# Kernel optimization log

Measured on AMD Instinct MI355X. Metric: run time of the kernel, lower is better.

The kernel has to match this reference:

```python
import jax, jax.numpy as jnp
import numpy as np

H, HKV, D, W = 64, 8, 64, 128          # heads, kv heads, head_dim, sliding window
G = H // HKV                            # query heads per kv head
HID = 2880
THETA = 150000.0
SCALE = D ** -0.5
NEG = -1e30


def _rope(x, positions):
    # x: [B,S,h,D]; GPT-NeoX style rotate_half RoPE
    half = D // 2
    inv_freq = 1.0 / (THETA ** (jnp.arange(0, half, dtype=jnp.float32) / half))
    ang = positions.astype(jnp.float32)[:, None] * inv_freq          # [S, D/2]
    cos = jnp.cos(ang)[None, :, None, :]
    sin = jnp.sin(ang)[None, :, None, :]
    x1, x2 = x[..., :half], x[..., half:]
    return jnp.concatenate([x1 * cos - x2 * sin, x2 * cos + x1 * sin], axis=-1)


def setup_inputs() -> dict:
    key = jax.random.key(0)
    ks = jax.random.split(key, 6)
    B, S = 1, 2048
    return {
        "hidden_states": jax.random.normal(ks[0], (B, S, HID), jnp.float32),
        "positions": jnp.arange(S, dtype=jnp.int32),
        "w_qkv": jax.random.normal(ks[1], (HID, (H + 2 * HKV) * D), jnp.float32) * 0.02,
        "b_qkv": jax.random.normal(ks[2], ((H + 2 * HKV) * D,), jnp.float32) * 0.02,
        "w_o": jax.random.normal(ks[3], (H * D, HID), jnp.float32) * 0.02,
        "b_o": jax.random.normal(ks[4], (HID,), jnp.float32) * 0.02,
        "sinks": jax.random.normal(ks[5], (H,), jnp.float32),
    }


def reference(hidden_states, positions, w_qkv, b_qkv, w_o, b_o, sinks):
    B, S, _ = hidden_states.shape
    qkv = hidden_states @ w_qkv + b_qkv                               # [B,S,(H+2Hkv)*D]
    q, k, v = jnp.split(qkv, [H * D, H * D + HKV * D], axis=-1)
    Q = q.reshape(B, S, H, D)
    K = k.reshape(B, S, HKV, D)
    V = v.reshape(B, S, HKV, D)
    Q = _rope(Q, positions)
    K = _rope(K, positions)

    # banded (sliding-window) key/value gather: query i sees keys i-W+1..i
    offsets = jnp.arange(W) - (W - 1)                                 # [-(W-1)..0]
    kidx = jnp.arange(S)[:, None] + offsets                           # [S,W]
    valid = kidx >= 0
    kidx = jnp.maximum(kidx, 0)
    Kw = K[:, kidx]                                                    # [B,S,W,HKV,D]
    Vw = V[:, kidx]

    Qr = Q.reshape(B, S, HKV, G, D)                                    # GQA grouping
    scores = jnp.einsum('bskgd,bswkd->bskgw', Qr, Kw) * SCALE          # [B,S,HKV,G,W]
    scores = jnp.where(valid[None, :, None, None, :], scores, NEG)

    sink = sinks.reshape(HKV, G)[None, None]                           # [1,1,HKV,G]
    m = jnp.maximum(scores.max(axis=-1), sink)                         # [B,S,HKV,G]
    p = jnp.exp(scores - m[..., None])
    denom = p.sum(axis=-1) + jnp.exp(sink - m)                         # sink in normalizer
    out = jnp.einsum('bskgw,bswkd->bskgd', p, Vw) / denom[..., None]

    out = out.reshape(B, S, H * D)
    return out @ w_o + b_o
```

## Files before the change

### kernel.cpp

```cpp
#include <hip/hip_runtime.h>

typedef unsigned short u16;
typedef __bf16 bf16x8 __attribute__((ext_vector_type(8)));
typedef float f32x4 __attribute__((ext_vector_type(4)));
typedef unsigned short u16x8 __attribute__((ext_vector_type(8)));

#define QKV_N 5120
#define SEQ 2048
#define ATTN_K 4096
#define KPAD 2944
#define SCALE 0.125f
#define NEGINF -1e30f

__device__ __forceinline__ u16 f2bf(float f) {
  unsigned int u = __builtin_bit_cast(unsigned int, f);
  u = (u + 0x7FFFu + ((u >> 16) & 1u)) >> 16;
  return (u16)u;
}

#define MFMA16(a, b, c) __builtin_amdgcn_mfma_f32_16x16x32_bf16((a), (b), (c), 0, 0, 0)

__device__ __forceinline__ void gl_lds16(const u16* g, u16* l) {
  __builtin_amdgcn_global_load_lds(
      (const __attribute__((address_space(1))) unsigned int*)(const void*)g,
      (__attribute__((address_space(3))) unsigned int*)(void*)l, 16, 0, 0);
}

__device__ __forceinline__ bf16x8 fragrd(const u16* base, int row, int rb) {
  return *(const bf16x8*)((const char*)(base + row * 32) + rb);
}

__device__ __forceinline__ bf16x8 lds_frag(const u16* mat, int row, int kh, int lg) {
  int off = row * 128 + ((kh * 64 + lg * 16) ^ ((row & 7) << 4));
  return *(const bf16x8*)((const char*)mat + off);
}

__global__ __launch_bounds__(256) void k_rope_table(const int* __restrict__ pos,
                                                    float2* __restrict__ tab) {
  int t = blockIdx.x * 256 + threadIdx.x;
  int s = t >> 5, i = t & 31;
  float freq = powf(150000.0f, -(float)i * (1.0f / 32.0f));
  float ang = (float)pos[s] * freq;
  float sv, cv;
  sincosf(ang, &sv, &cv);
  tab[t] = make_float2(cv, sv);
}

__global__ __launch_bounds__(256) void k_convert_pad(const float* __restrict__ in,
                                                     u16* __restrict__ out) {
  int i = blockIdx.x * 256 + threadIdx.x;
  int r = i / 736, c4 = i - r * 736;
  if (r >= 2048) return;
  ushort4 o = {0, 0, 0, 0};
  if (c4 < 720) {
    float4 v = *(const float4*)(in + (size_t)r * 2880 + c4 * 4);
    o.x = f2bf(v.x); o.y = f2bf(v.y); o.z = f2bf(v.z); o.w = f2bf(v.w);
  }
  ((ushort4*)out)[(size_t)r * 736 + c4] = o;
}

__global__ __launch_bounds__(256) void k_transpose(const float* __restrict__ in,
                                                   u16* __restrict__ out,
                                                   int Kin, int Kout, int Nd, int Npad) {
  __shared__ float tile[32][33];
  int n0 = blockIdx.x * 32, k0 = blockIdx.y * 32;
  int c = threadIdx.x & 31, r0 = threadIdx.x >> 5;
#pragma unroll
  for (int j = 0; j < 4; j++) {
    int r = r0 + j * 8;
    float v = 0.f;
    if (n0 + c < Nd && k0 + r < Kin) v = in[(size_t)(k0 + r) * Nd + n0 + c];
    tile[r][c] = v;
  }
  __syncthreads();
#pragma unroll
  for (int j = 0; j < 4; j++) {
    int rr = r0 + j * 8;
    int n = n0 + rr;
    if (n < Npad) out[(size_t)n * Kout + k0 + c] = f2bf(tile[c][rr]);
  }
}

__global__ __launch_bounds__(512, 1) void k_gemm1(const u16* __restrict__ Ag,
                                                  const u16* __restrict__ Bg,
                                                  const float* __restrict__ bias,
                                                  const float2* __restrict__ tab,
                                                  u16* __restrict__ C) {
  __shared__ u16 lds_[2][32768];
  u16* L = &lds_[0][0];
  const int tid = threadIdx.x;
  const int lane = tid & 63, wave = tid >> 6;
  const int wm = wave >> 2, wn = wave & 3;
  const int lr = lane & 15, lg = lane >> 4;
  int bid = blockIdx.x;
  int sb = (bid & 7) * 20 + (bid >> 3);
  const int m0 = (sb / 20) * 256, n0 = (sb % 20) * 256;

  f32x4 acc[8][4] = {};
  bf16x8 Bf[4];

  const int srow = wave * 16 + (lane >> 2);
  const int xsl = (((lane & 3) ^ ((lane >> 3) & 3)) << 3);
  const int rb = (lg * 16) ^ (((lr >> 1) & 3) << 4);

#define G1_STAGE_A(b, kh, kt)                                                   \
  { _Pragma("unroll") for (int r_ = 0; r_ < 2; r_++) {                          \
      gl_lds16(Ag + (size_t)(m0 + r_ * 128 + srow) * KPAD + (kt) + (kh) * 32 + xsl, \
               L + (b) * 32768 + (kh) * 8192 + (r_ * 128 + wave * 16) * 32); } }
#define G1_STAGE_B(b, kh, kt)                                                   \
  { _Pragma("unroll") for (int r_ = 0; r_ < 2; r_++) {                          \
      gl_lds16(Bg + (size_t)(n0 + r_ * 128 + srow) * KPAD + (kt) + (kh) * 32 + xsl, \
               L + (b) * 32768 + 16384 + (kh) * 8192 + (r_ * 128 + wave * 16) * 32); } }

#define VM4 asm volatile("s_waitcnt vmcnt(4)" ::: "memory");
#define VM0 asm volatile("s_waitcnt vmcnt(0)" ::: "memory");

#define PHASE(bb, kh, mh, LOADB, STAGE_STMT, WAIT_STMT)                         \
  {                                                                             \
    if (LOADB) {                                                                \
      _Pragma("unroll") for (int nf = 0; nf < 4; nf++)                          \
        Bf[nf] = fragrd(L + (bb) * 32768 + 16384 + (kh) * 8192,                 \
                        wn * 64 + nf * 16 + lr, rb);                            \
    }                                                                           \
    bf16x8 Af[4];                                                               \
    _Pragma("unroll") for (int mi = 0; mi < 4; mi++)                            \
      Af[mi] = fragrd(L + (bb) * 32768 + (kh) * 8192,                           \
                      wm * 128 + ((mh) * 4 + mi) * 16 + lr, rb);                \
    STAGE_STMT;                                                                 \
    WAIT_STMT;                                                                  \
    __builtin_amdgcn_s_barrier();                                               \
    __builtin_amdgcn_s_setprio(1);                                              \
    _Pragma("unroll") for (int mi = 0; mi < 4; mi++)                            \
      _Pragma("unroll") for (int nf = 0; nf < 4; nf++)                          \
        acc[(mh) * 4 + mi][nf] = MFMA16(Af[mi], Bf[nf], acc[(mh) * 4 + mi][nf]); \
    __builtin_amdgcn_s_setprio(0);                                              \
    __builtin_amdgcn_s_barrier();                                               \
  }

  G1_STAGE_A(0, 0, 0)
  G1_STAGE_B(0, 0, 0)
  G1_STAGE_A(0, 1, 0)
  G1_STAGE_B(0, 1, 0)
  VM4
  __builtin_amdgcn_s_barrier();

#define G1_ITER(ii, TAILV)                                                      \
  {                                                                             \
    const int ktB = (2 * (ii) + 1) * 64;                                        \
    const int ktC = (2 * (ii) + 2) * 64;                                        \
    PHASE(0, 0, 0, true,  { G1_STAGE_A(1, 0, ktB) }, {})                        \
    PHASE(0, 0, 1, false, { G1_STAGE_B(1, 0, ktB) }, VM4)                       \
    PHASE(0, 1, 0, true,  { G1_STAGE_A(1, 1, ktB) }, {})                        \
    PHASE(0, 1, 1, false, { G1_STAGE_B(1, 1, ktB) }, VM4)                       \
    PHASE(1, 0, 0, true,  { if (!(TAILV)) G1_STAGE_A(0, 0, ktC) }, {})          \
    PHASE(1, 0, 1, false, { if (!(TAILV)) G1_STAGE_B(0, 0, ktC) },              \
          { if (TAILV) { VM0 } else { VM4 } })                                  \
    PHASE(1, 1, 0, true,  { if (!(TAILV)) G1_STAGE_A(0, 1, ktC) }, {})          \
    PHASE(1, 1, 1, false, { if (!(TAILV)) G1_STAGE_B(0, 1, ktC) },              \
          { if (!(TAILV)) { VM4 } })                                            \
  }

  for (int i = 0; i < 22; i++) {
    G1_ITER(i, false)
  }
  G1_ITER(22, true)

#undef G1_ITER
#undef PHASE
#undef G1_STAGE_A
#undef G1_STAGE_B

  const bool rope = (n0 < 4608);
  if (rope) {
#pragma unroll
    for (int mf = 0; mf < 8; mf++)
#pragma unroll
      for (int nf = 0; nf < 2; nf++) {
        int col1 = n0 + wn * 64 + nf * 16 + lr;
        int col2 = col1 + 32;
        float b1 = bias[col1], b2 = bias[col2];
#pragma unroll
        for (int rg = 0; rg < 4; rg++) {
          int row = m0 + wm * 128 + mf * 16 + lg * 4 + rg;
          float2 cs = tab[(size_t)row * 32 + nf * 16 + lr];
          float x1 = acc[mf][nf][rg] + b1;
          float x2 = acc[mf][nf + 2][rg] + b2;
          C[(size_t)row * QKV_N + col1] = f2bf(x1 * cs.x - x2 * cs.y);
          C[(size_t)row * QKV_N + col2] = f2bf(x2 * cs.x + x1 * cs.y);
        }
      }
  } else {
#pragma unroll
    for (int mf = 0; mf < 8; mf++)
#pragma unroll
      for (int nf = 0; nf < 4; nf++) {
        int col = n0 + wn * 64 + nf * 16 + lr;
        float bv = bias[col];
#pragma unroll
        for (int rg = 0; rg < 4; rg++) {
          int row = m0 + wm * 128 + mf * 16 + lg * 4 + rg;
          C[(size_t)row * QKV_N + col] = f2bf(acc[mf][nf][rg] + bv);
        }
      }
  }
}

__global__ __launch_bounds__(256, 2) void k_gemm2(const u16* __restrict__ Ag,
                                                  const u16* __restrict__ Bg,
                                                  const float* __restrict__ bias,
                                                  float* __restrict__ C) {
  __shared__ u16 ldsbuf[2][16384];
  const int tid = threadIdx.x;
  const int lane = tid & 63, wave = tid >> 6;
  const int wm = wave >> 1, wn = wave & 1;
  const int lr = lane & 15, lg = lane >> 4;
  int bid = blockIdx.x;
  int sb = (bid & 7) * 46 + (bid >> 3);
  const int m0 = (sb / 23) * 128, n0 = (sb % 23) * 128;

  f32x4 acc[4][4] = {};

  const int srow = wave * 8 + (lane >> 3);
  const int sc = ((lane & 7) ^ (lane >> 3)) << 3;
  const u16* gA = Ag + (size_t)(m0 + srow) * ATTN_K + sc;
  const u16* gB = Bg + (size_t)(n0 + srow) * ATTN_K + sc;

#define G2_STAGE(kt, b)                                                          \
  {                                                                              \
    u16* Ab = &ldsbuf[b][0];                                                     \
    u16* Bb = &ldsbuf[b][8192];                                                  \
    _Pragma("unroll") for (int r = 0; r < 4; r++) {                              \
      gl_lds16(gA + (size_t)(r * 32) * ATTN_K + (kt), Ab + (r * 32 + wave * 8) * 64); \
      gl_lds16(gB + (size_t)(r * 32) * ATTN_K + (kt), Bb + (r * 32 + wave * 8) * 64); \
    }                                                                            \
  }

  G2_STAGE(0, 0)
  G2_STAGE(64, 1)
  asm volatile("s_waitcnt vmcnt(8)" ::: "memory");
  __builtin_amdgcn_s_barrier();

  for (int t = 0; t < 64; t++) {
    const int b = t & 1;
    const u16* La = &ldsbuf[b][0];
    const u16* Lb = &ldsbuf[b][8192];
    bf16x8 Bf[4][2];
#pragma unroll
    for (int nf = 0; nf < 4; nf++)
#pragma unroll
      for (int kh = 0; kh < 2; kh++)
        Bf[nf][kh] = lds_frag(Lb, wn * 64 + nf * 16 + lr, kh, lg);
    bf16x8 Af[2][2];
#pragma unroll
    for (int mi = 0; mi < 2; mi++)
#pragma unroll
      for (int kh = 0; kh < 2; kh++)
        Af[mi][kh] = lds_frag(La, wm * 64 + mi * 16 + lr, kh, lg);
#pragma unroll
    for (int q = 0; q < 2; q++) {
      bf16x8 An[2][2];
      if (q < 1) {
#pragma unroll
        for (int mi = 0; mi < 2; mi++)
#pragma unroll
          for (int kh = 0; kh < 2; kh++)
            An[mi][kh] = lds_frag(La, wm * 64 + ((q + 1) * 2 + mi) * 16 + lr, kh, lg);
      }
      __builtin_amdgcn_s_setprio(1);
#pragma unroll
      for (int mi = 0; mi < 2; mi++)
#pragma unroll
        for (int nf = 0; nf < 4; nf++)
#pragma unroll
          for (int kh = 0; kh < 2; kh++)
            acc[q * 2 + mi][nf] = MFMA16(Af[mi][kh], Bf[nf][kh], acc[q * 2 + mi][nf]);
      __builtin_amdgcn_s_setprio(0);
      if (q < 1) {
#pragma unroll
        for (int mi = 0; mi < 2; mi++)
#pragma unroll
          for (int kh = 0; kh < 2; kh++)
            Af[mi][kh] = An[mi][kh];
      }
    }
    __builtin_amdgcn_s_barrier();
    if (t <= 61) {
      G2_STAGE((t + 2) * 64, b)
      asm volatile("s_waitcnt vmcnt(8)" ::: "memory");
    } else {
      asm volatile("s_waitcnt vmcnt(0)" ::: "memory");
    }
    __builtin_amdgcn_s_barrier();
  }
#undef G2_STAGE

#pragma unroll
  for (int mi = 0; mi < 4; mi++)
#pragma unroll
    for (int ni = 0; ni < 4; ni++) {
      int row = m0 + wm * 64 + mi * 16 + lg * 4;
      int col = n0 + wn * 64 + ni * 16 + lr;
      if (col < 2880) {
        float bv = bias[col];
#pragma unroll
        for (int rg = 0; rg < 4; rg++)
          C[(size_t)(row + rg) * 2880 + col] = acc[mi][ni][rg] + bv;
      }
    }
}

__global__ __launch_bounds__(512, 2) void k_attn(const u16* __restrict__ qkv,
                                                 const float* __restrict__ sinks,
                                                 u16* __restrict__ out) {
  __shared__ u16 Klds[160 * 64];
  __shared__ u16 Vt[64 * 168];
  __shared__ u16 Pslab[8 * 32 * 40];
  const int hk = blockIdx.y;
  const int s0 = blockIdx.x * 32;
  const int kb = s0 - 127;
  const int tid = threadIdx.x;
  const int lane = tid & 63, w = tid >> 6;
  const int lr = lane & 15, lg = lane >> 4;

  for (int ch = tid; ch < 160 * 8; ch += 512) {
    int key = ch >> 3, c = ch & 7;
    int kidx = kb + key;
    u16x8 val = {0, 0, 0, 0, 0, 0, 0, 0};
    if (kidx >= 0 && kidx < SEQ)
      val = *(const u16x8*)(qkv + (size_t)kidx * QKV_N + 4096 + hk * 64 + c * 8);
    int off = (key * 128 + c * 16) ^ ((key & 7) << 4);
    *(u16x8*)((char*)Klds + off) = val;
  }
  for (int e4 = tid; e4 < 160 * 16; e4 += 512) {
    int key = e4 >> 4, d0 = (e4 & 15) * 4;
    int kidx = kb + key;
    ushort4 v = {0, 0, 0, 0};
    if (kidx >= 0 && kidx < SEQ)
      v = *(const ushort4*)(qkv + (size_t)kidx * QKV_N + 4608 + hk * 64 + d0);
    Vt[(d0 + 0) * 168 + key] = v.x;
    Vt[(d0 + 1) * 168 + key] = v.y;
    Vt[(d0 + 2) * 168 + key] = v.z;
    Vt[(d0 + 3) * 168 + key] = v.w;
  }

  const int head = hk * 8 + w;
  bf16x8 qf[2][2];
#pragma unroll
  for (int rt = 0; rt < 2; rt++)
#pragma unroll
    for (int ks = 0; ks < 2; ks++)
      qf[rt][ks] = *(const bf16x8*)(qkv + (size_t)(s0 + rt * 16 + lr) * QKV_N +
                                    head * 64 + ks * 32 + lg * 8);
  __syncthreads();

  f32x4 sc[2][10];
  f32x4 zz = {0.f, 0.f, 0.f, 0.f};
#pragma unroll
  for (int rt = 0; rt < 2; rt++)
#pragma unroll
    for (int nt = 0; nt < 10; nt++) sc[rt][nt] = zz;
#pragma unroll
  for (int nt = 0; nt < 10; nt++) {
    int key = nt * 16 + lr;
#pragma unroll
    for (int ks = 0; ks < 2; ks++) {
      int off = (key * 128 + ks * 64 + lg * 16) ^ ((key & 7) << 4);
      bf16x8 kf = *(const bf16x8*)((const char*)Klds + off);
      sc[0][nt] = MFMA16(qf[0][ks], kf, sc[0][nt]);
      sc[1][nt] = MFMA16(qf[1][ks], kf, sc[1][nt]);
    }
  }

#pragma unroll
  for (int rt = 0; rt < 2; rt++)
#pragma unroll
    for (int nt = 0; nt < 10; nt++)
#pragma unroll
      for (int rg = 0; rg < 4; rg++) {
        int qq = rt * 16 + lg * 4 + rg;
        int j = nt * 16 + lr;
        bool valid = (j >= qq) && (j <= qq + 127) && ((kb + j) >= 0);
        sc[rt][nt][rg] = valid ? sc[rt][nt][rg] * SCALE : NEGINF;
      }

  const float sink = sinks[head];
  float den[2][4];
#pragma unroll
  for (int rt = 0; rt < 2; rt++)
#pragma unroll
    for (int rg = 0; rg < 4; rg++) {
      float m = NEGINF;
#pragma unroll
      for (int nt = 0; nt < 10; nt++) m = fmaxf(m, sc[rt][nt][rg]);
#pragma unroll
      for (int x = 1; x < 16; x <<= 1) m = fmaxf(m, __shfl_xor(m, x, 64));
      m = fmaxf(m, sink);
      float sum = 0.f;
#pragma unroll
      for (int nt = 0; nt < 10; nt++) {
        float p = __expf(sc[rt][nt][rg] - m);
        sc[rt][nt][rg] = p;
        sum += p;
      }
#pragma unroll
      for (int x = 1; x < 16; x <<= 1) sum += __shfl_xor(sum, x, 64);
      den[rt][rg] = sum + __expf(sink - m);
    }

  f32x4 oacc[2][4];
#pragma unroll
  for (int rt = 0; rt < 2; rt++)
#pragma unroll
    for (int dn = 0; dn < 4; dn++) oacc[rt][dn] = zz;
  u16* slab = &Pslab[w * 32 * 40];
#pragma unroll
  for (int kt = 0; kt < 5; kt++) {
#pragma unroll
    for (int rt = 0; rt < 2; rt++)
#pragma unroll
      for (int j2 = 0; j2 < 2; j2++)
#pragma unroll
        for (int rg = 0; rg < 4; rg++)
          slab[(rt * 16 + lg * 4 + rg) * 40 + j2 * 16 + lr] = f2bf(sc[rt][kt * 2 + j2][rg]);
    asm volatile("s_waitcnt lgkmcnt(0)" ::: "memory");
    __builtin_amdgcn_sched_barrier(0);
    bf16x8 pf0 = *(const bf16x8*)&slab[lr * 40 + lg * 8];
    bf16x8 pf1 = *(const bf16x8*)&slab[(16 + lr) * 40 + lg * 8];
#pragma unroll
    for (int dn = 0; dn < 4; dn++) {
      bf16x8 vf = *(const bf16x8*)&Vt[(dn * 16 + lr) * 168 + kt * 32 + lg * 8];
      oacc[0][dn] = MFMA16(pf0, vf, oacc[0][dn]);
      oacc[1][dn] = MFMA16(pf1, vf, oacc[1][dn]);
    }
  }

#pragma unroll
  for (int rt = 0; rt < 2; rt++)
#pragma unroll
    for (int dn = 0; dn < 4; dn++)
#pragma unroll
      for (int rg = 0; rg < 4; rg++) {
        int s = s0 + rt * 16 + lg * 4 + rg;
        float val = oacc[rt][dn][rg] / den[rt][rg];
        out[(size_t)s * ATTN_K + head * 64 + dn * 16 + lr] = f2bf(val);
      }
}

extern "C" void kernel_launch(void* const* d_in, const int* in_sizes, int n_in,
                              void* d_out, int out_size, void* d_ws, size_t ws_size,
                              hipStream_t stream) {
  const float* hs = (const float*)d_in[0];
  const int* pos = (const int*)d_in[1];
  const float* wqkv = (const float*)d_in[2];
  const float* bqkv = (const float*)d_in[3];
  const float* wo = (const float*)d_in[4];
  const float* bo = (const float*)d_in[5];
  const float* sinks = (const float*)d_in[6];
  float* out = (float*)d_out;

  char* ws = (char*)d_ws;
  u16* qkvb = (u16*)(ws + 0);
  u16* hsb = (u16*)(ws + 41943040);
  u16* wqkvT = (u16*)(ws + 54001664);
  u16* attnb = (u16*)(ws + 41943040);
  u16* woT = (u16*)(ws + 84148224);
  float2* tab = (float2*)(ws + 108265472);

  k_rope_table<<<256, 256, 0, stream>>>(pos, tab);
  k_convert_pad<<<5888, 256, 0, stream>>>(hs, hsb);
  k_transpose<<<dim3(160, 92), 256, 0, stream>>>(wqkv, wqkvT, 2880, KPAD, 5120, 5120);
  k_transpose<<<dim3(92, 128), 256, 0, stream>>>(wo, woT, 4096, 4096, 2880, 2944);
  k_gemm1<<<160, 512, 0, stream>>>(hsb, wqkvT, bqkv, tab, qkvb);
  k_attn<<<dim3(64, 8), 512, 0, stream>>>(qkvb, sinks, attnb);
  k_gemm2<<<368, 256, 0, stream>>>(attnb, woT, bo, out);
}
```

Baseline: 202.2 us.

## Double-buffer LDS fragment reads in QKV GEMM to overlap with MFMAs

Restructures the QKV projection GEMM main loop so the A/B fragments for the next phase are read from LDS into alternating register sets while the current phase's MFMAs run. Before, each phase read its fragments and then immediately consumed them. The global-to-LDS staging and vmcnt waits are also regrouped, with A and B issued together in some phases. This is meant to hide LDS read latency behind matrix-core work. The cost is roughly double the fragment registers, plus a more intricate barrier and wait ordering that must stay correct.

```diff
diff --git a/kernel.cpp b/kernel.cpp
--- a/kernel.cpp
+++ b/kernel.cpp
@@ -97,7 +97,7 @@
   const int m0 = (sb / 20) * 256, n0 = (sb % 20) * 256;
 
   f32x4 acc[8][4] = {};
-  bf16x8 Bf[4];
+  bf16x8 AfA[4], AfB[4], BfA[4], BfB[4];
 
   const int srow = wave * 16 + (lane >> 2);
   const int xsl = (((lane & 3) ^ ((lane >> 3) & 3)) << 3);
@@ -115,24 +115,25 @@
 #define VM4 asm volatile("s_waitcnt vmcnt(4)" ::: "memory");
 #define VM0 asm volatile("s_waitcnt vmcnt(0)" ::: "memory");
 
-#define PHASE(bb, kh, mh, LOADB, STAGE_STMT, WAIT_STMT)                         \
+#define PREF_A(dst, bb, kh, mh)                                                 \
+  _Pragma("unroll") for (int mi = 0; mi < 4; mi++)                              \
+    dst[mi] = fragrd(L + (bb) * 32768 + (kh) * 8192,                            \
+                     wm * 128 + ((mh) * 4 + mi) * 16 + lr, rb);
+#define PREF_B(dst, bb, kh)                                                     \
+  _Pragma("unroll") for (int nf = 0; nf < 4; nf++)                              \
+    dst[nf] = fragrd(L + (bb) * 32768 + 16384 + (kh) * 8192,                    \
+                     wn * 64 + nf * 16 + lr, rb);
+
+#define PH(STAGE_STMT, WAIT_STMT, PREF_STMT, mh, AFS, BFS)                      \
   {                                                                             \
-    if (LOADB) {                                                                \
-      _Pragma("unroll") for (int nf = 0; nf < 4; nf++)                          \
-        Bf[nf] = fragrd(L + (bb) * 32768 + 16384 + (kh) * 8192,                 \
-                        wn * 64 + nf * 16 + lr, rb);                            \
-    }                                                                           \
-    bf16x8 Af[4];                                                               \
-    _Pragma("unroll") for (int mi = 0; mi < 4; mi++)                            \
-      Af[mi] = fragrd(L + (bb) * 32768 + (kh) * 8192,                           \
-                      wm * 128 + ((mh) * 4 + mi) * 16 + lr, rb);                \
     STAGE_STMT;                                                                 \
+    PREF_STMT;                                                                  \
     WAIT_STMT;                                                                  \
     __builtin_amdgcn_s_barrier();                                               \
     __builtin_amdgcn_s_setprio(1);                                              \
     _Pragma("unroll") for (int mi = 0; mi < 4; mi++)                            \
       _Pragma("unroll") for (int nf = 0; nf < 4; nf++)                          \
-        acc[(mh) * 4 + mi][nf] = MFMA16(Af[mi], Bf[nf], acc[(mh) * 4 + mi][nf]); \
+        acc[(mh) * 4 + mi][nf] = MFMA16(AFS[mi], BFS[nf], acc[(mh) * 4 + mi][nf]); \
     __builtin_amdgcn_s_setprio(0);                                              \
     __builtin_amdgcn_s_barrier();                                               \
   }
@@ -143,21 +144,32 @@
   G1_STAGE_B(0, 1, 0)
   VM4
   __builtin_amdgcn_s_barrier();
+  PREF_A(AfA, 0, 0, 0)
+  PREF_B(BfA, 0, 0)
 
 #define G1_ITER(ii, TAILV)                                                      \
   {                                                                             \
     const int ktB = (2 * (ii) + 1) * 64;                                        \
     const int ktC = (2 * (ii) + 2) * 64;                                        \
-    PHASE(0, 0, 0, true,  { G1_STAGE_A(1, 0, ktB) }, {})                        \
-    PHASE(0, 0, 1, false, { G1_STAGE_B(1, 0, ktB) }, VM4)                       \
-    PHASE(0, 1, 0, true,  { G1_STAGE_A(1, 1, ktB) }, {})                        \
-    PHASE(0, 1, 1, false, { G1_STAGE_B(1, 1, ktB) }, VM4)                       \
-    PHASE(1, 0, 0, true,  { if (!(TAILV)) G1_STAGE_A(0, 0, ktC) }, {})          \
-    PHASE(1, 0, 1, false, { if (!(TAILV)) G1_STAGE_B(0, 0, ktC) },              \
-          { if (TAILV) { VM0 } else { VM4 } })                                  \
-    PHASE(1, 1, 0, true,  { if (!(TAILV)) G1_STAGE_A(0, 1, ktC) }, {})          \
-    PHASE(1, 1, 1, false, { if (!(TAILV)) G1_STAGE_B(0, 1, ktC) },              \
-          { if (!(TAILV)) { VM4 } })                                            \
+     PH({ G1_STAGE_A(1, 0, ktB) G1_STAGE_B(1, 0, ktB) }, VM4,             \
+              { PREF_A(AfB, 0, 0, 1) }, 0, AfA, BfA)                            \
+     PH({ G1_STAGE_A(1, 1, ktB) }, {},                                    \
+              { PREF_A(AfA, 0, 1, 0) PREF_B(BfB, 0, 1) }, 1, AfB, BfA)          \
+     PH({ G1_STAGE_B(1, 1, ktB) }, VM4,                                   \
+              { PREF_A(AfB, 0, 1, 1) }, 0, AfA, BfB)                            \
+     PH({ if (!(TAILV)) G1_STAGE_A(0, 0, ktC) }, {},                      \
+              { PREF_A(AfA, 1, 0, 0) PREF_B(BfA, 1, 0) }, 1, AfB, BfB)          \
+     PH({ if (!(TAILV)) G1_STAGE_B(0, 0, ktC) },                          \
+              { if (TAILV) { VM0 } else { VM4 } },                              \
+              { PREF_A(AfB, 1, 0, 1) }, 0, AfA, BfA)                            \
+     PH({ if (!(TAILV)) G1_STAGE_A(0, 1, ktC) }, {},                      \
+              { PREF_A(AfA, 1, 1, 0) PREF_B(BfB, 1, 1) }, 1, AfB, BfA)          \
+     PH({ if (!(TAILV)) G1_STAGE_B(0, 1, ktC) },                          \
+              { if (!(TAILV)) { VM4 } },                                        \
+              { PREF_A(AfB, 1, 1, 1) }, 0, AfA, BfB)                            \
+     PH({}, {},                                                           \
+              { if (!(TAILV)) { PREF_A(AfA, 0, 0, 0) PREF_B(BfA, 0, 0) } },     \
+              1, AfB, BfB)                                                      \
   }
 
   for (int i = 0; i < 22; i++) {
@@ -166,7 +178,9 @@
   G1_ITER(22, true)
 
 #undef G1_ITER
-#undef PHASE
+#undef PH
+#undef PREF_A
+#undef PREF_B
 #undef G1_STAGE_A
 #undef G1_STAGE_B
 
```

Measured after the change: 209.7 us. +3.7%, slower.

## Retile QKV GEMM to 128x160 blocks and move RoPE into attention

Applied to the files above, without the earlier changes.

The QKV projection GEMM moves from 160 blocks of 256x256 tiles with 512 threads to 512 blocks of 128x160 tiles with 256 threads and two blocks per CU. This fills all CUs on the 256-CU part instead of leaving wave quantization idle. RoPE leaves the GEMM epilogue, so the attention kernel now rotates K while staging it to LDS and rotates Q fragments after loading them. The cost is a bf16 round trip before rotation, which slightly changes numerics, plus extra ALU work in attention because each K row is rotated once per query block.

```diff
diff --git a/kernel.cpp b/kernel.cpp
--- a/kernel.cpp
+++ b/kernel.cpp
@@ -16,6 +16,10 @@
   unsigned int u = __builtin_bit_cast(unsigned int, f);
   u = (u + 0x7FFFu + ((u >> 16) & 1u)) >> 16;
   return (u16)u;
+}
+__device__ __forceinline__ float bf2f(u16 u) {
+  unsigned int x = ((unsigned int)u) << 16;
+  return __builtin_bit_cast(float, x);
 }
 
 #define MFMA16(a, b, c) __builtin_amdgcn_mfma_f32_16x16x32_bf16((a), (b), (c), 0, 0, 0)
@@ -81,128 +85,104 @@
   }
 }
 
-__global__ __launch_bounds__(512, 1) void k_gemm1(const u16* __restrict__ Ag,
+__global__ __launch_bounds__(256, 2) void k_gemm1(const u16* __restrict__ Ag,
                                                   const u16* __restrict__ Bg,
                                                   const float* __restrict__ bias,
-                                                  const float2* __restrict__ tab,
                                                   u16* __restrict__ C) {
-  __shared__ u16 lds_[2][32768];
+  __shared__ u16 lds_[2][18432];
   u16* L = &lds_[0][0];
   const int tid = threadIdx.x;
   const int lane = tid & 63, wave = tid >> 6;
-  const int wm = wave >> 2, wn = wave & 3;
+  const int wm = wave >> 1, wn = wave & 1;
   const int lr = lane & 15, lg = lane >> 4;
-  int bid = blockIdx.x;
-  int sb = (bid & 7) * 20 + (bid >> 3);
-  const int m0 = (sb / 20) * 256, n0 = (sb % 20) * 256;
-
-  f32x4 acc[8][4] = {};
-  bf16x8 Bf[4];
-
-  const int srow = wave * 16 + (lane >> 2);
-  const int xsl = (((lane & 3) ^ ((lane >> 3) & 3)) << 3);
+  const int bid = blockIdx.x;
+  const int sb = (bid & 7) * 64 + (bid >> 3);
+  const int m0 = (sb >> 5) * 128, n0 = (sb & 31) * 160;
+
+  f32x4 acc[4][5] = {};
+  bf16x8 Bf[5], Af0, Af1;
+
   const int rb = (lg * 16) ^ (((lr >> 1) & 3) << 4);
-
-#define G1_STAGE_A(b, kh, kt)                                                   \
-  { _Pragma("unroll") for (int r_ = 0; r_ < 2; r_++) {                          \
-      gl_lds16(Ag + (size_t)(m0 + r_ * 128 + srow) * KPAD + (kt) + (kh) * 32 + xsl, \
-               L + (b) * 32768 + (kh) * 8192 + (r_ * 128 + wave * 16) * 32); } }
-#define G1_STAGE_B(b, kh, kt)                                                   \
-  { _Pragma("unroll") for (int r_ = 0; r_ < 2; r_++) {                          \
-      gl_lds16(Bg + (size_t)(n0 + r_ * 128 + srow) * KPAD + (kt) + (kh) * 32 + xsl, \
-               L + (b) * 32768 + 16384 + (kh) * 8192 + (r_ * 128 + wave * 16) * 32); } }
-
+  const int arow = tid >> 2;
+  const int axs = ((tid & 3) ^ ((tid >> 3) & 3)) << 3;
+
+  size_t boff[5];
+#pragma unroll
+  for (int r_ = 0; r_ < 5; r_++) {
+    int e = r_ * 2048 + tid * 8;
+    int bkh = (e >= 5120) ? 1 : 0;
+    int re = e - bkh * 5120;
+    int brow = re >> 5;
+    int bch = (re >> 3) & 3;
+    int bps = bch ^ ((brow >> 1) & 3);
+    boff[r_] = (size_t)(n0 + brow) * KPAD + bkh * 32 + bps * 8;
+  }
+
+#define STA(b, kh, kt, r_)                                                      \
+  gl_lds16(Ag + (size_t)(m0 + (r_) * 64 + arow) * KPAD + (kt) + (kh) * 32 + axs, \
+           L + (b) * 18432 + (kh) * 4096 + (r_) * 2048 + wave * 512)
+#define STB(b, kt, r_)                                                          \
+  gl_lds16(Bg + boff[r_] + (kt), L + (b) * 18432 + 8192 + (r_) * 2048 + wave * 512)
+#define RDB(b, kh)                                                              \
+  { _Pragma("unroll") for (int nf = 0; nf < 5; nf++)                            \
+      Bf[nf] = fragrd(L + (b) * 18432 + 8192 + (kh) * 5120,                     \
+                      wn * 80 + nf * 16 + lr, rb); }
+#define RDA(b, kh, mf0_)                                                        \
+  { Af0 = fragrd(L + (b) * 18432 + (kh) * 4096, wm * 64 + (mf0_) * 16 + lr, rb); \
+    Af1 = fragrd(L + (b) * 18432 + (kh) * 4096, wm * 64 + ((mf0_) + 1) * 16 + lr, rb); }
+#define MM(ma, mb)                                                              \
+  { __builtin_amdgcn_s_setprio(1);                                              \
+    _Pragma("unroll") for (int nf = 0; nf < 5; nf++) {                          \
+      acc[ma][nf] = MFMA16(Af0, Bf[nf], acc[ma][nf]);                           \
+      acc[mb][nf] = MFMA16(Af1, Bf[nf], acc[mb][nf]); }                         \
+    __builtin_amdgcn_s_setprio(0); }
+#define BAR __builtin_amdgcn_s_barrier();
 #define VM4 asm volatile("s_waitcnt vmcnt(4)" ::: "memory");
 #define VM0 asm volatile("s_waitcnt vmcnt(0)" ::: "memory");
 
-#define PHASE(bb, kh, mh, LOADB, STAGE_STMT, WAIT_STMT)                         \
-  {                                                                             \
-    if (LOADB) {                                                                \
-      _Pragma("unroll") for (int nf = 0; nf < 4; nf++)                          \
-        Bf[nf] = fragrd(L + (bb) * 32768 + 16384 + (kh) * 8192,                 \
-                        wn * 64 + nf * 16 + lr, rb);                            \
-    }                                                                           \
-    bf16x8 Af[4];                                                               \
-    _Pragma("unroll") for (int mi = 0; mi < 4; mi++)                            \
-      Af[mi] = fragrd(L + (bb) * 32768 + (kh) * 8192,                           \
-                      wm * 128 + ((mh) * 4 + mi) * 16 + lr, rb);                \
-    STAGE_STMT;                                                                 \
-    WAIT_STMT;                                                                  \
-    __builtin_amdgcn_s_barrier();                                               \
-    __builtin_amdgcn_s_setprio(1);                                              \
-    _Pragma("unroll") for (int mi = 0; mi < 4; mi++)                            \
-      _Pragma("unroll") for (int nf = 0; nf < 4; nf++)                          \
-        acc[(mh) * 4 + mi][nf] = MFMA16(Af[mi], Bf[nf], acc[(mh) * 4 + mi][nf]); \
-    __builtin_amdgcn_s_setprio(0);                                              \
-    __builtin_amdgcn_s_barrier();                                               \
-  }
-
-  G1_STAGE_A(0, 0, 0)
-  G1_STAGE_B(0, 0, 0)
-  G1_STAGE_A(0, 1, 0)
-  G1_STAGE_B(0, 1, 0)
-  VM4
-  __builtin_amdgcn_s_barrier();
-
-#define G1_ITER(ii, TAILV)                                                      \
-  {                                                                             \
-    const int ktB = (2 * (ii) + 1) * 64;                                        \
-    const int ktC = (2 * (ii) + 2) * 64;                                        \
-    PHASE(0, 0, 0, true,  { G1_STAGE_A(1, 0, ktB) }, {})                        \
-    PHASE(0, 0, 1, false, { G1_STAGE_B(1, 0, ktB) }, VM4)                       \
-    PHASE(0, 1, 0, true,  { G1_STAGE_A(1, 1, ktB) }, {})                        \
-    PHASE(0, 1, 1, false, { G1_STAGE_B(1, 1, ktB) }, VM4)                       \
-    PHASE(1, 0, 0, true,  { if (!(TAILV)) G1_STAGE_A(0, 0, ktC) }, {})          \
-    PHASE(1, 0, 1, false, { if (!(TAILV)) G1_STAGE_B(0, 0, ktC) },              \
-          { if (TAILV) { VM0 } else { VM4 } })                                  \
-    PHASE(1, 1, 0, true,  { if (!(TAILV)) G1_STAGE_A(0, 1, ktC) }, {})          \
-    PHASE(1, 1, 1, false, { if (!(TAILV)) G1_STAGE_B(0, 1, ktC) },              \
-          { if (!(TAILV)) { VM4 } })                                            \
-  }
-
-  for (int i = 0; i < 22; i++) {
-    G1_ITER(i, false)
-  }
-  G1_ITER(22, true)
-
-#undef G1_ITER
-#undef PHASE
-#undef G1_STAGE_A
-#undef G1_STAGE_B
-
-  const bool rope = (n0 < 4608);
-  if (rope) {
-#pragma unroll
-    for (int mf = 0; mf < 8; mf++)
-#pragma unroll
-      for (int nf = 0; nf < 2; nf++) {
-        int col1 = n0 + wn * 64 + nf * 16 + lr;
-        int col2 = col1 + 32;
-        float b1 = bias[col1], b2 = bias[col2];
-#pragma unroll
-        for (int rg = 0; rg < 4; rg++) {
-          int row = m0 + wm * 128 + mf * 16 + lg * 4 + rg;
-          float2 cs = tab[(size_t)row * 32 + nf * 16 + lr];
-          float x1 = acc[mf][nf][rg] + b1;
-          float x2 = acc[mf][nf + 2][rg] + b2;
-          C[(size_t)row * QKV_N + col1] = f2bf(x1 * cs.x - x2 * cs.y);
-          C[(size_t)row * QKV_N + col2] = f2bf(x2 * cs.x + x1 * cs.y);
-        }
-      }
-  } else {
-#pragma unroll
-    for (int mf = 0; mf < 8; mf++)
-#pragma unroll
-      for (int nf = 0; nf < 4; nf++) {
-        int col = n0 + wn * 64 + nf * 16 + lr;
-        float bv = bias[col];
-#pragma unroll
-        for (int rg = 0; rg < 4; rg++) {
-          int row = m0 + wm * 128 + mf * 16 + lg * 4 + rg;
-          C[(size_t)row * QKV_N + col] = f2bf(acc[mf][nf][rg] + bv);
-        }
-      }
-  }
+  STA(0, 0, 0, 0); STA(0, 0, 0, 1);
+  STB(0, 0, 0); STB(0, 0, 1); STB(0, 0, 2); STB(0, 0, 3); STB(0, 0, 4);
+  STA(0, 1, 0, 0); STA(0, 1, 0, 1);
+  VM4 BAR
+
+  for (int t = 0; t < 46; t++) {
+    const int b = t & 1, nb = b ^ 1;
+    const int kt1 = (t + 1) * 64;
+    const bool st = (t < 45);
+    RDB(b, 0) RDA(b, 0, 0)
+    if (st) { STA(nb, 0, kt1, 0); STA(nb, 0, kt1, 1); STB(nb, kt1, 0); }
+    BAR MM(0, 1) BAR
+    RDA(b, 0, 2)
+    if (st) { STB(nb, kt1, 1); STB(nb, kt1, 2); VM4 } else { VM0 }
+    BAR MM(2, 3) BAR
+    RDB(b, 1) RDA(b, 1, 0)
+    if (st) { STB(nb, kt1, 3); STB(nb, kt1, 4); }
+    BAR MM(0, 1) BAR
+    RDA(b, 1, 2)
+    if (st) { STA(nb, 1, kt1, 0); STA(nb, 1, kt1, 1); VM4 }
+    BAR MM(2, 3) BAR
+  }
+#undef STA
+#undef STB
+#undef RDB
+#undef RDA
+#undef MM
+#undef BAR
+#undef VM4
+#undef VM0
+
+#pragma unroll
+  for (int mf = 0; mf < 4; mf++)
+#pragma unroll
+    for (int nf = 0; nf < 5; nf++) {
+      int col = n0 + wn * 80 + nf * 16 + lr;
+      float bv = bias[col];
+#pragma unroll
+      for (int rg = 0; rg < 4; rg++) {
+        int row = m0 + wm * 64 + mf * 16 + lg * 4 + rg;
+        C[(size_t)row * QKV_N + col] = f2bf(acc[mf][nf][rg] + bv);
+      }
+    }
 }
 
 __global__ __launch_bounds__(256, 2) void k_gemm2(const u16* __restrict__ Ag,
@@ -311,6 +291,7 @@
 
 __global__ __launch_bounds__(512, 2) void k_attn(const u16* __restrict__ qkv,
                                                  const float* __restrict__ sinks,
+                                                 const float2* __restrict__ tab,
                                                  u16* __restrict__ out) {
   __shared__ u16 Klds[160 * 64];
   __shared__ u16 Vt[64 * 168];
@@ -322,14 +303,27 @@
   const int lane = tid & 63, w = tid >> 6;
   const int lr = lane & 15, lg = lane >> 4;
 
-  for (int ch = tid; ch < 160 * 8; ch += 512) {
-    int key = ch >> 3, c = ch & 7;
+  for (int u = tid; u < 160 * 4; u += 512) {
+    int key = u >> 2, c = u & 3;
     int kidx = kb + key;
-    u16x8 val = {0, 0, 0, 0, 0, 0, 0, 0};
-    if (kidx >= 0 && kidx < SEQ)
-      val = *(const u16x8*)(qkv + (size_t)kidx * QKV_N + 4096 + hk * 64 + c * 8);
-    int off = (key * 128 + c * 16) ^ ((key & 7) << 4);
-    *(u16x8*)((char*)Klds + off) = val;
+    u16x8 v1 = {0, 0, 0, 0, 0, 0, 0, 0}, v2 = v1;
+    if (kidx >= 0 && kidx < SEQ) {
+      const u16* base = qkv + (size_t)kidx * QKV_N + 4096 + hk * 64;
+      u16x8 x1 = *(const u16x8*)(base + c * 8);
+      u16x8 x2 = *(const u16x8*)(base + 32 + c * 8);
+      const float2* cs = tab + (size_t)kidx * 32 + c * 8;
+#pragma unroll
+      for (int j = 0; j < 8; j++) {
+        float f1 = bf2f(x1[j]), f2 = bf2f(x2[j]);
+        float2 t = cs[j];
+        v1[j] = f2bf(f1 * t.x - f2 * t.y);
+        v2[j] = f2bf(f2 * t.x + f1 * t.y);
+      }
+    }
+    int o1 = (key * 128 + c * 16) ^ ((key & 7) << 4);
+    int o2 = (key * 128 + (c + 4) * 16) ^ ((key & 7) << 4);
+    *(u16x8*)((char*)Klds + o1) = v1;
+    *(u16x8*)((char*)Klds + o2) = v2;
   }
   for (int e4 = tid; e4 < 160 * 16; e4 += 512) {
     int key = e4 >> 4, d0 = (e4 & 15) * 4;
@@ -346,11 +340,23 @@
   const int head = hk * 8 + w;
   bf16x8 qf[2][2];
 #pragma unroll
-  for (int rt = 0; rt < 2; rt++)
-#pragma unroll
-    for (int ks = 0; ks < 2; ks++)
-      qf[rt][ks] = *(const bf16x8*)(qkv + (size_t)(s0 + rt * 16 + lr) * QKV_N +
-                                    head * 64 + ks * 32 + lg * 8);
+  for (int rt = 0; rt < 2; rt++) {
+    int s = s0 + rt * 16 + lr;
+    const u16* base = qkv + (size_t)s * QKV_N + head * 64 + lg * 8;
+    u16x8 r0 = *(const u16x8*)(base);
+    u16x8 r1 = *(const u16x8*)(base + 32);
+    const float2* cs = tab + (size_t)s * 32 + lg * 8;
+    u16x8 y0, y1;
+#pragma unroll
+    for (int j = 0; j < 8; j++) {
+      float f1 = bf2f(r0[j]), f2 = bf2f(r1[j]);
+      float2 t = cs[j];
+      y0[j] = f2bf(f1 * t.x - f2 * t.y);
+      y1[j] = f2bf(f2 * t.x + f1 * t.y);
+    }
+    qf[rt][0] = __builtin_bit_cast(bf16x8, y0);
+    qf[rt][1] = __builtin_bit_cast(bf16x8, y1);
+  }
   __syncthreads();
 
   f32x4 sc[2][10];
@@ -470,7 +476,7 @@
   k_convert_pad<<<5888, 256, 0, stream>>>(hs, hsb);
   k_transpose<<<dim3(160, 92), 256, 0, stream>>>(wqkv, wqkvT, 2880, KPAD, 5120, 5120);
   k_transpose<<<dim3(92, 128), 256, 0, stream>>>(wo, woT, 4096, 4096, 2880, 2944);
-  k_gemm1<<<160, 512, 0, stream>>>(hsb, wqkvT, bqkv, tab, qkvb);
-  k_attn<<<dim3(64, 8), 512, 0, stream>>>(qkvb, sinks, attnb);
+  k_gemm1<<<512, 256, 0, stream>>>(hsb, wqkvT, bqkv, qkvb);
+  k_attn<<<dim3(64, 8), 512, 0, stream>>>(qkvb, sinks, tab, attnb);
   k_gemm2<<<368, 256, 0, stream>>>(attnb, woT, bo, out);
 }
```

Measured after the change: 202.3 us. No clear change (+0.0%).
